# Kernel tuning notes

Measured on AMD Instinct MI355X. Metric: run time of the kernel, lower is better.

## Reference

```python
import jax, jax.numpy as jnp
import numpy as np

B, QUE, VAL, D = 4, 128, 128, 512

def setup_inputs() -> dict:
    key = jax.random.key(0)
    k = jax.random.split(key, 8)
    return {
        "qs_1": jax.random.normal(k[0], (B, QUE, D), jnp.float32),
        "qs_2": jax.random.normal(k[1], (B, QUE, D), jnp.float32),  # unused by forward, kept for signature fidelity
        "ks":   jax.random.normal(k[2], (B, VAL, D), jnp.float32),
        "vs":   jax.random.normal(k[3], (B, VAL, D), jnp.float32),
        "sg_mask": jax.random.randint(k[4], (B, VAL), 0, 2).astype(bool),  # True = masked
        "W1":  jax.random.normal(k[5], (D, D), jnp.float32) / np.sqrt(D),
        "b1":  jnp.zeros((D,), jnp.float32),
        "Wse": jax.random.normal(k[6], (D, D), jnp.float32) / np.sqrt(D),
        "bse": jnp.zeros((D,), jnp.float32),
        "W2":  jax.random.normal(k[7], (D, 1), jnp.float32) / np.sqrt(D),
        "b2":  jnp.zeros((1,), jnp.float32),
    }

def reference(qs_1, qs_2, ks, vs, sg_mask, W1, b1, Wse, bse, W2, b2):
    # Pairwise query-key elementwise product: [B, que, val, d]
    x = qs_1[:, :, None, :] * ks[:, None, :, :]
    # linear1: Linear(d,d) + ReLU (dropout = identity at eval)
    h = jax.nn.relu(jnp.einsum('bqvd,de->bqve', x, W1) + b1)
    # linear2: Linear(d,1) + ReLU -> scalar score per (q, v) pair
    s = jax.nn.relu(jnp.einsum('bqvd,do->bqvo', h, W2) + b2)[..., 0]  # [B, que, val]
    m = sg_mask[:, None, :]                      # [B, 1, val], True = masked out
    # masked mean of h over the val axis (masked_fill(0) then divide by valid count)
    h = jnp.where(m[..., None], 0.0, h)
    denom = jnp.sum(~sg_mask, axis=-1).astype(h.dtype)      # [B]
    mean = h.sum(axis=2) / denom[:, None, None]             # [B, que, d]
    # squeeze-excitation gate: sigmoid(relu(Linear(d,d)))
    gate = jax.nn.sigmoid(jax.nn.relu(mean @ Wse + bse))    # [B, que, d]
    # masked softmax over val, weighted sum of values
    s = jnp.where(m, -1e9, s)
    w = jax.nn.softmax(s, axis=-1)                          # [B, que, val]
    out = jnp.einsum('bqv,bvd->bqd', w, vs)                 # [B, que, d]
    return gate * out
```

## Files before the change

### kernel.cpp

```cpp
#include <hip/hip_runtime.h>
#include <stdint.h>
#include <stddef.h>

#define BDIM 4
#define QUE  128
#define VAL  128
#define DD   512
#define BQ   (BDIM*QUE)
#define BK   32
#define SROW(r) ((((r) + ((r) >> 2))) & 3)

typedef float    f32x4 __attribute__((ext_vector_type(4)));
typedef float    f32x2 __attribute__((ext_vector_type(2)));
typedef _Float16 f16x8 __attribute__((ext_vector_type(8)));
typedef _Float16 f16x4 __attribute__((ext_vector_type(4)));
typedef _Float16 f16x2 __attribute__((ext_vector_type(2)));

typedef const __attribute__((address_space(1))) void* gas_ptr;
typedef __attribute__((address_space(3))) void*       las_ptr;

__device__ __forceinline__ void async_copy16(const void* g, void* l) {
    __builtin_amdgcn_global_load_lds((gas_ptr)g, (las_ptr)l, 16, 0, 0);
}

__global__ __launch_bounds__(256) void prep_kernel(const float* __restrict__ W1,
                                                   _Float16* __restrict__ W1T,
                                                   const float* __restrict__ Wse,
                                                   _Float16* __restrict__ WseH) {
    if (blockIdx.y < 16) {
        __shared__ float tile[32][33];
        int tx = threadIdx.x & 31;
        int ty = threadIdx.x >> 5;
        int d0 = blockIdx.x * 32;
        int e0 = blockIdx.y * 32;
        #pragma unroll
        for (int r = 0; r < 4; ++r)
            tile[ty + r*8][tx] = W1[(size_t)(d0 + ty + r*8) * DD + e0 + tx];
        __syncthreads();
        #pragma unroll
        for (int r = 0; r < 4; ++r) {
            int el = ty + r*8;
            W1T[(size_t)(e0 + el) * DD + d0 + tx] = (_Float16)tile[tx][el];
        }
    } else {
        size_t base = (size_t)blockIdx.x * 16384 + threadIdx.x * 4;
        #pragma unroll 4
        for (int i = 0; i < 16; ++i) {
            f32x4 w = *(const f32x4*)(Wse + base + (size_t)i * 1024);
            f16x4 h;
            h[0] = (_Float16)w[0]; h[1] = (_Float16)w[1];
            h[2] = (_Float16)w[2]; h[3] = (_Float16)w[3];
            *(f16x4*)(WseH + base + (size_t)i * 1024) = h;
        }
    }
}

__global__ __launch_bounds__(512, 4) void gemm_h_kernel(
    const float* __restrict__ qs1,
    const float* __restrict__ ks,
    const int*   __restrict__ sgmask,
    const _Float16* __restrict__ W1T,
    const float* __restrict__ b1,
    const float* __restrict__ W2,
    float* __restrict__ s_part,
    float* __restrict__ meansum)
{
    __shared__ _Float16 Ah[128 * BK];
    __shared__ _Float16 Bh[256 * BK];
    __shared__ float qrow[DD];
    __shared__ float sred[4][VAL];
    __shared__ float msumLDS[2][256];

    const int tid  = threadIdx.x;
    const int bq   = blockIdx.x;
    const int gy   = blockIdx.y;
    const int b    = bq >> 7;
    const int lane = tid & 63;
    const int wid  = tid >> 6;
    const int wm   = wid >> 2;
    const int wn   = wid & 3;
    const int quad = lane >> 4;
    const int lr   = lane & 15;

    if (tid < 128)
        *(f32x4*)(qrow + tid * 4) = *(const f32x4*)(qs1 + (size_t)bq * DD + tid * 4);

    f32x4 acc[4][4];
    #pragma unroll
    for (int i = 0; i < 4; ++i)
        #pragma unroll
        for (int j = 0; j < 4; ++j) acc[i][j] = (f32x4){0.f, 0.f, 0.f, 0.f};

    const int r4 = tid >> 2;
    const int cs = tid & 3;
    const int ca = (cs - SROW(r4)) & 3;
    const float* ksrow = ks + ((size_t)b * VAL + r4) * DD + ca * 8;
    const float* qbase = qrow + ca * 8;
    _Float16* a_dst = &Ah[r4 * BK + cs * 8];
    const int rb1 = 128 + r4;
    const int cb0 = (cs - SROW(r4)) & 3;
    const int cb1 = (cs - SROW(rb1)) & 3;
    const _Float16* gB0 = W1T + (size_t)(gy * 256 + r4) * DD + cb0 * 8;
    const _Float16* gB1 = W1T + (size_t)(gy * 256 + rb1) * DD + cb1 * 8;
    _Float16* ldsB0 = &Bh[(wid * 16) * BK];
    _Float16* ldsB1 = &Bh[(128 + wid * 16) * BK];

    const _Float16* fa_ptr[4];
    const _Float16* fb_ptr[4];
    #pragma unroll
    for (int mt = 0; mt < 4; ++mt) {
        int row = wm * 64 + mt * 16 + lr;
        fa_ptr[mt] = &Ah[row * BK + ((quad + SROW(row)) & 3) * 8];
    }
    #pragma unroll
    for (int nt = 0; nt < 4; ++nt) {
        int row = wn * 64 + nt * 16 + lr;
        fb_ptr[nt] = &Bh[row * BK + ((quad + SROW(row)) & 3) * 8];
    }
    __syncthreads();

    for (int kk = 0; kk < DD; kk += BK) {
        async_copy16(gB0 + kk, ldsB0);
        async_copy16(gB1 + kk, ldsB1);
        f32x4 kv0 = *(const f32x4*)(ksrow + kk);
        f32x4 kv1 = *(const f32x4*)(ksrow + kk + 4);
        f32x4 qv0 = *(const f32x4*)(qbase + kk);
        f32x4 qv1 = *(const f32x4*)(qbase + kk + 4);
        f16x8 av;
        #pragma unroll
        for (int c = 0; c < 4; ++c) {
            av[c]     = (_Float16)(kv0[c] * qv0[c]);
            av[c + 4] = (_Float16)(kv1[c] * qv1[c]);
        }
        *(f16x8*)a_dst = av;
        __syncthreads();

        f16x8 fa[4];
        #pragma unroll
        for (int mt = 0; mt < 4; ++mt) fa[mt] = *(const f16x8*)fa_ptr[mt];
        #pragma unroll
        for (int nt = 0; nt < 4; ++nt) {
            f16x8 fb = *(const f16x8*)fb_ptr[nt];
            #pragma unroll
            for (int mt = 0; mt < 4; ++mt)
                acc[mt][nt] = __builtin_amdgcn_mfma_f32_16x16x32_f16(fa[mt], fb, acc[mt][nt], 0, 0, 0);
        }
        __syncthreads();
    }

    float b1v[4], w2v[4];
    #pragma unroll
    for (int nt = 0; nt < 4; ++nt) {
        int col = gy*256 + wn*64 + nt*16 + lr;
        b1v[nt] = b1[col];
        w2v[nt] = W2[col];
    }
    float msum[4] = {0.f, 0.f, 0.f, 0.f};
    #pragma unroll
    for (int mt = 0; mt < 4; ++mt) {
        #pragma unroll
        for (int reg = 0; reg < 4; ++reg) {
            int v = wm*64 + mt*16 + quad*4 + reg;
            int masked = sgmask[b * VAL + v];
            float sacc = 0.f;
            #pragma unroll
            for (int nt = 0; nt < 4; ++nt) {
                float h = acc[mt][nt][reg] + b1v[nt];
                h = fmaxf(h, 0.f);
                sacc += h * w2v[nt];
                if (!masked) msum[nt] += h;
            }
            sacc += __shfl_xor(sacc, 1);
            sacc += __shfl_xor(sacc, 2);
            sacc += __shfl_xor(sacc, 4);
            sacc += __shfl_xor(sacc, 8);
            if (lr == 0) sred[wn][v] = sacc;
        }
    }
    #pragma unroll
    for (int nt = 0; nt < 4; ++nt) {
        float m = msum[nt];
        m += __shfl_xor(m, 16);
        m += __shfl_xor(m, 32);
        if (lane < 16) msumLDS[wm][wn*64 + nt*16 + lr] = m;
    }
    __syncthreads();
    if (tid < 128) {
        s_part[((size_t)bq * 2 + gy) * VAL + tid] =
            sred[0][tid] + sred[1][tid] + sred[2][tid] + sred[3][tid];
    } else if (tid >= 256) {
        int c = tid - 256;
        meansum[(size_t)bq * DD + gy*256 + c] = msumLDS[0][c] + msumLDS[1][c];
    }
}

__global__ __launch_bounds__(256) void finish_kernel(
    const float* __restrict__ s_part,
    const float* __restrict__ meansum,
    const int*   __restrict__ sgmask,
    const float* __restrict__ vs,
    const _Float16* __restrict__ WseH,
    const float* __restrict__ bse,
    const float* __restrict__ b2,
    float* __restrict__ out)
{
    __shared__ float wexp[VAL];
    __shared__ float meanLDS[DD];
    __shared__ float gred[4][128];
    __shared__ float ored[4][128];
    __shared__ float redv[2];
    const int tid = threadIdx.x;
    const int bq  = blockIdx.x;
    const int dt  = blockIdx.y;
    const int b   = bq >> 7;

    meanLDS[tid]       = meansum[(size_t)bq * DD + tid];
    meanLDS[tid + 256] = meansum[(size_t)bq * DD + tid + 256];

    if (tid < 64) {
        int v0 = tid, v1 = tid + 64;
        const float* sp = s_part + (size_t)bq * 2 * VAL;
        float s0 = fmaxf(sp[v0] + sp[VAL + v0] + b2[0], 0.f);
        float s1 = fmaxf(sp[v1] + sp[VAL + v1] + b2[0], 0.f);
        int m0 = sgmask[b * VAL + v0], m1 = sgmask[b * VAL + v1];
        float cnt = (m0 ? 0.f : 1.f) + (m1 ? 0.f : 1.f);
        if (m0) s0 = -1e9f;
        if (m1) s1 = -1e9f;
        float mx = fmaxf(s0, s1);
        #pragma unroll
        for (int off = 32; off; off >>= 1) mx = fmaxf(mx, __shfl_xor(mx, off));
        float e0 = __expf(s0 - mx), e1 = __expf(s1 - mx);
        float se = e0 + e1;
        #pragma unroll
        for (int off = 32; off; off >>= 1) {
            se  += __shfl_xor(se, off);
            cnt += __shfl_xor(cnt, off);
        }
        wexp[v0] = e0;  wexp[v1] = e1;
        if (tid == 0) { redv[0] = 1.f / se; redv[1] = 1.f / cnt; }
    }
    __syncthreads();

    const int dp = tid & 63;
    const int q4 = tid >> 6;
    const int d0 = dt * 128 + dp * 2;

    float g0 = 0.f, g1 = 0.f;
    const _Float16* wp = WseH + (size_t)(q4 * 128) * DD + d0;
    const float*    mp = meanLDS + q4 * 128;
    #pragma unroll 8
    for (int e = 0; e < 128; ++e) {
        f16x2 w = *(const f16x2*)(wp + (size_t)e * DD);
        float m = mp[e];
        g0 += m * (float)w[0];
        g1 += m * (float)w[1];
    }
    *(f32x2*)&gred[q4][dp * 2] = (f32x2){g0, g1};

    float o0 = 0.f, o1 = 0.f;
    const float* vp = vs + ((size_t)b * VAL + q4 * 32) * DD + d0;
    const float* wx = wexp + q4 * 32;
    #pragma unroll 8
    for (int v = 0; v < 32; ++v) {
        f32x2 vv = *(const f32x2*)(vp + (size_t)v * DD);
        o0 += wx[v] * vv[0];
        o1 += wx[v] * vv[1];
    }
    *(f32x2*)&ored[q4][dp * 2] = (f32x2){o0, o1};
    __syncthreads();

    if (tid < 128) {
        int d = dt * 128 + tid;
        float gate = (gred[0][tid] + gred[1][tid] + gred[2][tid] + gred[3][tid]) * redv[1] + bse[d];
        gate = fmaxf(gate, 0.f);
        gate = 1.f / (1.f + __expf(-gate));
        float o = ored[0][tid] + ored[1][tid] + ored[2][tid] + ored[3][tid];
        out[(size_t)bq * DD + d] = gate * o * redv[0];
    }
}

extern "C" void kernel_launch(void* const* d_in, const int* in_sizes, int n_in,
                              void* d_out, int out_size, void* d_ws, size_t ws_size,
                              hipStream_t stream) {
    (void)in_sizes; (void)n_in; (void)out_size; (void)ws_size;
    const float* qs1 = (const float*)d_in[0];
    const float* ks  = (const float*)d_in[2];
    const float* vs  = (const float*)d_in[3];
    const int*   sg  = (const int*)d_in[4];
    const float* W1  = (const float*)d_in[5];
    const float* b1  = (const float*)d_in[6];
    const float* Wse = (const float*)d_in[7];
    const float* bse = (const float*)d_in[8];
    const float* W2  = (const float*)d_in[9];
    const float* b2  = (const float*)d_in[10];
    float* out = (float*)d_out;

    char* ws = (char*)d_ws;
    _Float16* W1T    = (_Float16*)ws;
    _Float16* WseH   = (_Float16*)(ws + (512 << 10));
    float*    s_part = (float*)(ws + (1 << 20));
    float*    msum   = (float*)(ws + (1 << 20) + (512 << 10));

    prep_kernel<<<dim3(16, 17), 256, 0, stream>>>(W1, W1T, Wse, WseH);
    gemm_h_kernel<<<dim3(BQ, 2), 512, 0, stream>>>(qs1, ks, sg, W1T, b1, W2, s_part, msum);
    finish_kernel<<<dim3(BQ, 4), 256, 0, stream>>>(s_part, msum, sg, vs, WseH, bse, b2, out);
}
```

Before: 145.5 us.

## Replace scalar finish stage with MFMA-based gate and value GEMMs

Splits the old finish kernel into a small mid kernel and a final kernel. The mid kernel computes the normalized softmax weights and the mean, storing both as fp16. The final kernel computes mean@Wse and w@vs with 16x16x32 fp16 MFMA tiles over 32 queries by 64 columns. Prep now also transposes Wse and vs into fp16. This removes the per-(bq, d-tile) redundant scalar reads of Wse and vs, at the cost of an extra launch, fp16 rounding of the softmax weights and values, and only 128 single-wave blocks in the final kernel.

```diff
diff --git a/kernel.cpp b/kernel.cpp
--- a/kernel.cpp
+++ b/kernel.cpp
@@ -26,31 +26,44 @@
 __global__ __launch_bounds__(256) void prep_kernel(const float* __restrict__ W1,
                                                    _Float16* __restrict__ W1T,
                                                    const float* __restrict__ Wse,
-                                                   _Float16* __restrict__ WseH) {
-    if (blockIdx.y < 16) {
-        __shared__ float tile[32][33];
-        int tx = threadIdx.x & 31;
-        int ty = threadIdx.x >> 5;
-        int d0 = blockIdx.x * 32;
-        int e0 = blockIdx.y * 32;
+                                                   _Float16* __restrict__ WseT,
+                                                   const float* __restrict__ vs,
+                                                   _Float16* __restrict__ vsT) {
+    __shared__ float tile[32][33];
+    const int tx = threadIdx.x & 31;
+    const int ty = threadIdx.x >> 5;
+    const int gx = blockIdx.x, gy = blockIdx.y;
+    if (gy < 32) {
+        const float* src = (gy < 16) ? W1  : Wse;
+        _Float16*    dst = (gy < 16) ? W1T : WseT;
+        int a0 = gx * 32;
+        int b0 = (gy & 15) * 32;
         #pragma unroll
         for (int r = 0; r < 4; ++r)
-            tile[ty + r*8][tx] = W1[(size_t)(d0 + ty + r*8) * DD + e0 + tx];
+            tile[ty + r*8][tx] = src[(size_t)(a0 + ty + r*8) * DD + b0 + tx];
         __syncthreads();
         #pragma unroll
         for (int r = 0; r < 4; ++r) {
             int el = ty + r*8;
-            W1T[(size_t)(e0 + el) * DD + d0 + tx] = (_Float16)tile[tx][el];
+            dst[(size_t)(b0 + el) * DD + a0 + tx] = (_Float16)tile[tx][el];
         }
     } else {
-        size_t base = (size_t)blockIdx.x * 16384 + threadIdx.x * 4;
-        #pragma unroll 4
-        for (int i = 0; i < 16; ++i) {
-            f32x4 w = *(const f32x4*)(Wse + base + (size_t)i * 1024);
-            f16x4 h;
-            h[0] = (_Float16)w[0]; h[1] = (_Float16)w[1];
-            h[2] = (_Float16)w[2]; h[3] = (_Float16)w[3];
-            *(f16x4*)(WseH + base + (size_t)i * 1024) = h;
+        int bb = gy - 32;
+        const float* src = vs  + (size_t)bb * VAL * DD;
+        _Float16*    dst = vsT + (size_t)bb * DD * VAL;
+        int b0 = gx * 32;
+        for (int vt = 0; vt < 4; ++vt) {
+            int a0 = vt * 32;
+            __syncthreads();
+            #pragma unroll
+            for (int r = 0; r < 4; ++r)
+                tile[ty + r*8][tx] = src[(size_t)(a0 + ty + r*8) * DD + b0 + tx];
+            __syncthreads();
+            #pragma unroll
+            for (int r = 0; r < 4; ++r) {
+                int el = ty + r*8;
+                dst[(size_t)(b0 + el) * VAL + a0 + tx] = (_Float16)tile[tx][el];
+            }
         }
     }
 }
@@ -98,9 +111,8 @@
     const float* qbase = qrow + ca * 8;
     _Float16* a_dst = &Ah[r4 * BK + cs * 8];
     const int rb1 = 128 + r4;
-    const int cb0 = (cs - SROW(r4)) & 3;
     const int cb1 = (cs - SROW(rb1)) & 3;
-    const _Float16* gB0 = W1T + (size_t)(gy * 256 + r4) * DD + cb0 * 8;
+    const _Float16* gB0 = W1T + (size_t)(gy * 256 + r4) * DD + ca * 8;
     const _Float16* gB1 = W1T + (size_t)(gy * 256 + rb1) * DD + cb1 * 8;
     _Float16* ldsB0 = &Bh[(wid * 16) * BK];
     _Float16* ldsB1 = &Bh[(128 + wid * 16) * BK];
@@ -194,88 +206,118 @@
     }
 }
 
-__global__ __launch_bounds__(256) void finish_kernel(
+__global__ __launch_bounds__(64) void mid_kernel(
     const float* __restrict__ s_part,
     const float* __restrict__ meansum,
     const int*   __restrict__ sgmask,
-    const float* __restrict__ vs,
-    const _Float16* __restrict__ WseH,
+    const float* __restrict__ b2,
+    _Float16* __restrict__ wH,
+    _Float16* __restrict__ meanH)
+{
+    const int bq = blockIdx.x;
+    const int b  = bq >> 7;
+    const int lane = threadIdx.x;
+    const float* sp = s_part + (size_t)bq * 2 * VAL;
+    float s0 = fmaxf(sp[lane]      + sp[128 + lane]      + b2[0], 0.f);
+    float s1 = fmaxf(sp[64 + lane] + sp[192 + lane]      + b2[0], 0.f);
+    int m0 = sgmask[b * VAL + lane], m1 = sgmask[b * VAL + 64 + lane];
+    float cnt = (m0 ? 0.f : 1.f) + (m1 ? 0.f : 1.f);
+    if (m0) s0 = -1e9f;
+    if (m1) s1 = -1e9f;
+    float mx = fmaxf(s0, s1);
+    #pragma unroll
+    for (int off = 32; off; off >>= 1) mx = fmaxf(mx, __shfl_xor(mx, off));
+    float e0 = __expf(s0 - mx), e1 = __expf(s1 - mx);
+    float se = e0 + e1;
+    #pragma unroll
+    for (int off = 32; off; off >>= 1) {
+        se  += __shfl_xor(se, off);
+        cnt += __shfl_xor(cnt, off);
+    }
+    float invse = 1.f / se;
+    float invd  = 1.f / cnt;
+    f16x2 wv; wv[0] = (_Float16)(e0 * invse); wv[1] = (_Float16)(e1 * invse);
+    wH[(size_t)bq * VAL + lane]      = wv[0];
+    wH[(size_t)bq * VAL + 64 + lane] = wv[1];
+    f32x4 mA = *(const f32x4*)(meansum + (size_t)bq * DD + lane * 8);
+    f32x4 mB = *(const f32x4*)(meansum + (size_t)bq * DD + lane * 8 + 4);
+    f16x8 mh;
+    #pragma unroll
+    for (int c = 0; c < 4; ++c) {
+        mh[c]     = (_Float16)(mA[c] * invd);
+        mh[c + 4] = (_Float16)(mB[c] * invd);
+    }
+    *(f16x8*)(meanH + (size_t)bq * DD + lane * 8) = mh;
+}
+
+__global__ __launch_bounds__(64) void final_kernel(
+    const _Float16* __restrict__ meanH,
+    const _Float16* __restrict__ WseT,
+    const _Float16* __restrict__ wH,
+    const _Float16* __restrict__ vsT,
     const float* __restrict__ bse,
-    const float* __restrict__ b2,
     float* __restrict__ out)
 {
-    __shared__ float wexp[VAL];
-    __shared__ float meanLDS[DD];
-    __shared__ float gred[4][128];
-    __shared__ float ored[4][128];
-    __shared__ float redv[2];
-    const int tid = threadIdx.x;
-    const int bq  = blockIdx.x;
-    const int dt  = blockIdx.y;
-    const int b   = bq >> 7;
-
-    meanLDS[tid]       = meansum[(size_t)bq * DD + tid];
-    meanLDS[tid + 256] = meansum[(size_t)bq * DD + tid + 256];
-
-    if (tid < 64) {
-        int v0 = tid, v1 = tid + 64;
-        const float* sp = s_part + (size_t)bq * 2 * VAL;
-        float s0 = fmaxf(sp[v0] + sp[VAL + v0] + b2[0], 0.f);
-        float s1 = fmaxf(sp[v1] + sp[VAL + v1] + b2[0], 0.f);
-        int m0 = sgmask[b * VAL + v0], m1 = sgmask[b * VAL + v1];
-        float cnt = (m0 ? 0.f : 1.f) + (m1 ? 0.f : 1.f);
-        if (m0) s0 = -1e9f;
-        if (m1) s1 = -1e9f;
-        float mx = fmaxf(s0, s1);
-        #pragma unroll
-        for (int off = 32; off; off >>= 1) mx = fmaxf(mx, __shfl_xor(mx, off));
-        float e0 = __expf(s0 - mx), e1 = __expf(s1 - mx);
-        float se = e0 + e1;
-        #pragma unroll
-        for (int off = 32; off; off >>= 1) {
-            se  += __shfl_xor(se, off);
-            cnt += __shfl_xor(cnt, off);
-        }
-        wexp[v0] = e0;  wexp[v1] = e1;
-        if (tid == 0) { redv[0] = 1.f / se; redv[1] = 1.f / cnt; }
-    }
-    __syncthreads();
-
-    const int dp = tid & 63;
-    const int q4 = tid >> 6;
-    const int d0 = dt * 128 + dp * 2;
-
-    float g0 = 0.f, g1 = 0.f;
-    const _Float16* wp = WseH + (size_t)(q4 * 128) * DD + d0;
-    const float*    mp = meanLDS + q4 * 128;
-    #pragma unroll 8
-    for (int e = 0; e < 128; ++e) {
-        f16x2 w = *(const f16x2*)(wp + (size_t)e * DD);
-        float m = mp[e];
-        g0 += m * (float)w[0];
-        g1 += m * (float)w[1];
-    }
-    *(f32x2*)&gred[q4][dp * 2] = (f32x2){g0, g1};
-
-    float o0 = 0.f, o1 = 0.f;
-    const float* vp = vs + ((size_t)b * VAL + q4 * 32) * DD + d0;
-    const float* wx = wexp + q4 * 32;
-    #pragma unroll 8
-    for (int v = 0; v < 32; ++v) {
-        f32x2 vv = *(const f32x2*)(vp + (size_t)v * DD);
-        o0 += wx[v] * vv[0];
-        o1 += wx[v] * vv[1];
-    }
-    *(f32x2*)&ored[q4][dp * 2] = (f32x2){o0, o1};
-    __syncthreads();
-
-    if (tid < 128) {
-        int d = dt * 128 + tid;
-        float gate = (gred[0][tid] + gred[1][tid] + gred[2][tid] + gred[3][tid]) * redv[1] + bse[d];
-        gate = fmaxf(gate, 0.f);
-        gate = 1.f / (1.f + __expf(-gate));
-        float o = ored[0][tid] + ored[1][tid] + ored[2][tid] + ored[3][tid];
-        out[(size_t)bq * DD + d] = gate * o * redv[0];
+    const int lane = threadIdx.x;
+    const int lr   = lane & 15;
+    const int quad = lane >> 4;
+    const int q0   = blockIdx.x * 32;
+    const int d0   = blockIdx.y * 64;
+    const int b    = q0 >> 7;
+
+    f32x4 ga[2][4], oa[2][4];
+    #pragma unroll
+    for (int i = 0; i < 2; ++i)
+        #pragma unroll
+        for (int j = 0; j < 4; ++j) { ga[i][j] = (f32x4){0,0,0,0}; oa[i][j] = (f32x4){0,0,0,0}; }
+
+    const _Float16* ap0 = meanH + (size_t)(q0 + lr) * DD + quad * 8;
+    const _Float16* bp0 = WseT  + (size_t)(d0 + lr) * DD + quad * 8;
+    #pragma unroll 2
+    for (int kk = 0; kk < DD; kk += 32) {
+        f16x8 am[2];
+        #pragma unroll
+        for (int mt = 0; mt < 2; ++mt)
+            am[mt] = *(const f16x8*)(ap0 + (size_t)mt * 16 * DD + kk);
+        #pragma unroll
+        for (int nt = 0; nt < 4; ++nt) {
+            f16x8 bw = *(const f16x8*)(bp0 + (size_t)nt * 16 * DD + kk);
+            #pragma unroll
+            for (int mt = 0; mt < 2; ++mt)
+                ga[mt][nt] = __builtin_amdgcn_mfma_f32_16x16x32_f16(am[mt], bw, ga[mt][nt], 0, 0, 0);
+        }
+    }
+    const _Float16* wp0 = wH  + (size_t)(q0 + lr) * VAL + quad * 8;
+    const _Float16* vp0 = vsT + (size_t)b * DD * VAL + (size_t)(d0 + lr) * VAL + quad * 8;
+    #pragma unroll
+    for (int kk = 0; kk < VAL; kk += 32) {
+        f16x8 am[2];
+        #pragma unroll
+        for (int mt = 0; mt < 2; ++mt)
+            am[mt] = *(const f16x8*)(wp0 + (size_t)mt * 16 * VAL + kk);
+        #pragma unroll
+        for (int nt = 0; nt < 4; ++nt) {
+            f16x8 bv = *(const f16x8*)(vp0 + (size_t)nt * 16 * VAL + kk);
+            #pragma unroll
+            for (int mt = 0; mt < 2; ++mt)
+                oa[mt][nt] = __builtin_amdgcn_mfma_f32_16x16x32_f16(am[mt], bv, oa[mt][nt], 0, 0, 0);
+        }
+    }
+    #pragma unroll
+    for (int nt = 0; nt < 4; ++nt) {
+        int col = d0 + nt * 16 + lr;
+        float bsev = bse[col];
+        #pragma unroll
+        for (int mt = 0; mt < 2; ++mt) {
+            #pragma unroll
+            for (int reg = 0; reg < 4; ++reg) {
+                int row = q0 + mt * 16 + quad * 4 + reg;
+                float garg = ga[mt][nt][reg] + bsev;
+                garg = fmaxf(garg, 0.f);
+                float gate = 1.f / (1.f + __expf(-garg));
+                out[(size_t)row * DD + col] = gate * oa[mt][nt][reg];
+            }
+        }
     }
 }
 
@@ -296,12 +338,16 @@
     float* out = (float*)d_out;
 
     char* ws = (char*)d_ws;
-    _Float16* W1T    = (_Float16*)ws;
-    _Float16* WseH   = (_Float16*)(ws + (512 << 10));
-    float*    s_part = (float*)(ws + (1 << 20));
-    float*    msum   = (float*)(ws + (1 << 20) + (512 << 10));
-
-    prep_kernel<<<dim3(16, 17), 256, 0, stream>>>(W1, W1T, Wse, WseH);
+    _Float16* W1T    = (_Float16*)(ws);
+    _Float16* WseT   = (_Float16*)(ws + (512 << 10));
+    _Float16* vsT    = (_Float16*)(ws + (1 << 20));
+    float*    s_part = (float*)(ws + (1536 << 10));
+    float*    msum   = (float*)(ws + (2 << 20));
+    _Float16* wH     = (_Float16*)(ws + (3 << 20));
+    _Float16* meanH  = (_Float16*)(ws + (3 << 20) + (128 << 10));
+
+    prep_kernel<<<dim3(16, 36), 256, 0, stream>>>(W1, W1T, Wse, WseT, vs, vsT);
     gemm_h_kernel<<<dim3(BQ, 2), 512, 0, stream>>>(qs1, ks, sg, W1T, b1, W2, s_part, msum);
-    finish_kernel<<<dim3(BQ, 4), 256, 0, stream>>>(s_part, msum, sg, vs, WseH, bse, b2, out);
-}
+    mid_kernel<<<BQ, 64, 0, stream>>>(s_part, msum, sg, b2, wH, meanH);
+    final_kernel<<<dim3(16, 8), 64, 0, stream>>>(meanH, WseT, wH, vsT, bse, out);
+}
```

New measurement: 139.2 us. 1.05x faster.
